# Kernel optimization log

Measured on AMD Instinct MI355X. Metric: run time of the kernel, lower is better.

Reference implementation:

```python
import jax, jax.numpy as jnp
import numpy as np

N = 200000      # num nodes
TOPK = 32       # PPR neighbors kept per node
EMB = 64        # embedding dim


def setup_inputs() -> dict:
    key = jax.random.key(0)
    k1, k2, k3 = jax.random.split(key, 3)
    emb_table = jax.random.normal(k1, (N, EMB), dtype=jnp.float32)
    wei = jax.random.uniform(k2, (N, TOPK), dtype=jnp.float32)
    nei = jax.random.randint(k3, (N, TOPK), 0, N, dtype=jnp.int64)
    return {"emb_table": emb_table, "wei": wei, "nei": nei}


def reference(emb_table, wei, nei):
    # Weight preprocessing from __init__: binary mask of nonzero ppr weights,
    # row-normalized -> uniform weights over valid neighbors.
    w = jnp.where(wei == 0, 0.0, 1.0)                       # [N, topk]
    w = w / (jnp.sum(w, axis=-1, keepdims=True) + 1e-12)    # [N, topk]
    # forward: gather neighbor embeddings, weighted sum over topk.
    top_embs = emb_table[nei]                                # [N, topk, emb]
    out = jnp.einsum("nk,nke->ne", w, top_embs)             # [N, emb]
    return out[:, None, :]                                   # [N, 1, emb] like matmul(w[:,None,:], top_embs)
```

## Files before the change

kernel.cpp:

```cpp
#include <hip/hip_runtime.h>

#define TOPK 32
#define EMB 64

__global__ __launch_bounds__(256) void absmax_partial_kernel(
    const float* __restrict__ emb, float* __restrict__ partial, int total4)
{
    const float4* src = (const float4*)emb;
    float m = 0.0f;
    for (int i = blockIdx.x * 256 + threadIdx.x; i < total4; i += gridDim.x * 256) {
        float4 v = src[i];
        m = fmaxf(m, fmaxf(fmaxf(fabsf(v.x), fabsf(v.y)),
                           fmaxf(fabsf(v.z), fabsf(v.w))));
    }
    __shared__ float red[256];
    red[threadIdx.x] = m;
    __syncthreads();
    for (int s = 128; s > 0; s >>= 1) {
        if (threadIdx.x < s) red[threadIdx.x] = fmaxf(red[threadIdx.x], red[threadIdx.x + s]);
        __syncthreads();
    }
    if (threadIdx.x == 0) partial[blockIdx.x] = red[0];
}

__global__ __launch_bounds__(256) void quant_kernel(
    const float* __restrict__ emb, signed char* __restrict__ emb8,
    const float* __restrict__ partial, float* __restrict__ stepOut,
    int n_nodes, int a_blocks)
{
    const int t = threadIdx.x;
    __shared__ float red[256];
    float m = fmaxf(fmaxf(partial[t], partial[t + 256]),
                    fmaxf(partial[t + 512], partial[t + 768]));
    red[t] = m;
    __syncthreads();
    for (int s = 128; s > 0; s >>= 1) {
        if (t < s) red[t] = fmaxf(red[t], red[t + s]);
        __syncthreads();
    }
    const float maxv = fmaxf(red[0], 1e-20f);
    const float inv_step = 127.0f / maxv;

    if ((int)blockIdx.x < a_blocks) {
        const int gid = blockIdx.x * 256 + t;
        const int total16 = n_nodes * (EMB / 16);
        if (gid < total16) {
            const float4* src = (const float4*)emb + (size_t)gid * 4;
            unsigned int w[4];
            #pragma unroll
            for (int p = 0; p < 4; ++p) {
                float4 v = src[p];
                int q0 = (int)__builtin_rintf(fminf(fmaxf(v.x * inv_step, -127.f), 127.f));
                int q1 = (int)__builtin_rintf(fminf(fmaxf(v.y * inv_step, -127.f), 127.f));
                int q2 = (int)__builtin_rintf(fminf(fmaxf(v.z * inv_step, -127.f), 127.f));
                int q3 = (int)__builtin_rintf(fminf(fmaxf(v.w * inv_step, -127.f), 127.f));
                w[p] = (unsigned int)(q0 & 0xff) | ((unsigned int)(q1 & 0xff) << 8) |
                       ((unsigned int)(q2 & 0xff) << 16) | ((unsigned int)(q3 & 0xff) << 24);
            }
            ((int4*)emb8)[gid] = make_int4((int)w[0], (int)w[1], (int)w[2], (int)w[3]);
        }
    } else {
        if (t < 4)
            ((int4*)(emb8 + (size_t)n_nodes * EMB))[t] = make_int4(0, 0, 0, 0);
        if (t == 0) stepOut[0] = maxv / 127.0f;
    }
}

__global__ __launch_bounds__(256) void gather_q8_kernel(
    const signed char* __restrict__ emb8,
    const float* __restrict__ wei,
    const int*   __restrict__ nei,
    const float* __restrict__ stepPtr,
    float*       __restrict__ out,
    int n_nodes)
{
    const int tid  = blockIdx.x * 256 + threadIdx.x;
    const int n    = tid >> 3;
    const int lane = tid & 7;
    if (n >= n_nodes) return;

    const float step = stepPtr[0];
    const long base = (long)n * TOPK;
    const int4   j4 = *(const int4*)(nei + base + lane * 4);
    const float4 w4 = *(const float4*)(wei + base + lane * 4);
    int jm[4];
    jm[0] = (w4.x != 0.0f) ? j4.x : n_nodes;
    jm[1] = (w4.y != 0.0f) ? j4.y : n_nodes;
    jm[2] = (w4.z != 0.0f) ? j4.z : n_nodes;
    jm[3] = (w4.w != 0.0f) ? j4.w : n_nodes;

    int acc[8] = {0, 0, 0, 0, 0, 0, 0, 0};
    int cnt = 0;

    #pragma unroll
    for (int t2 = 0; t2 < 4; ++t2) {
        int j[8];
        #pragma unroll
        for (int k = 0; k < 8; ++k)
            j[k] = __shfl(jm[k & 3], t2 * 2 + (k >> 2), 8);
        uint2 r[8];
        #pragma unroll
        for (int k = 0; k < 8; ++k)
            r[k] = *(const uint2*)(emb8 + (size_t)j[k] * EMB + lane * 8);
        #pragma unroll
        for (int k = 0; k < 8; ++k) {
            cnt += (j[k] != n_nodes) ? 1 : 0;
            const unsigned int x = r[k].x, y = r[k].y;
            acc[0] += (int)(signed char)(x & 0xff);
            acc[1] += (int)(signed char)((x >> 8) & 0xff);
            acc[2] += (int)(signed char)((x >> 16) & 0xff);
            acc[3] += ((int)x) >> 24;
            acc[4] += (int)(signed char)(y & 0xff);
            acc[5] += (int)(signed char)((y >> 8) & 0xff);
            acc[6] += (int)(signed char)((y >> 16) & 0xff);
            acc[7] += ((int)y) >> 24;
        }
    }

    const float mlt = step / ((float)cnt + 1e-12f);
    float4 o0, o1;
    o0.x = acc[0] * mlt; o0.y = acc[1] * mlt; o0.z = acc[2] * mlt; o0.w = acc[3] * mlt;
    o1.x = acc[4] * mlt; o1.y = acc[5] * mlt; o1.z = acc[6] * mlt; o1.w = acc[7] * mlt;
    float* op = out + (size_t)n * EMB + lane * 8;
    *(float4*)op       = o0;
    *(float4*)(op + 4) = o1;
}

__global__ __launch_bounds__(256) void pprgo_f32_kernel(
    const float* __restrict__ emb,
    const float* __restrict__ wei,
    const int*   __restrict__ nei,
    float*       __restrict__ out,
    int n_nodes)
{
    const int tid   = blockIdx.x * blockDim.x + threadIdx.x;
    const int group = tid >> 4;
    const int lane  = tid & 15;
    if (group >= n_nodes) return;
    const long base = (long)group * TOPK;
    const float w0 = wei[base + lane];
    const float w1 = wei[base + 16 + lane];
    const int   i0 = nei[base + lane];
    const int   i1 = nei[base + 16 + lane];
    const float m0 = (w0 != 0.0f) ? 1.0f : 0.0f;
    const float m1 = (w1 != 0.0f) ? 1.0f : 0.0f;
    float4 acc = make_float4(0.f, 0.f, 0.f, 0.f);
    float  cnt = 0.0f;
    #pragma unroll 8
    for (int k = 0; k < 16; ++k) {
        const int   j0 = __shfl(i0, k, 16);
        const float a0 = __shfl(m0, k, 16);
        const float4 r0 = *(const float4*)(emb + (size_t)j0 * EMB + lane * 4);
        acc.x += a0*r0.x; acc.y += a0*r0.y; acc.z += a0*r0.z; acc.w += a0*r0.w; cnt += a0;
        const int   j1 = __shfl(i1, k, 16);
        const float a1 = __shfl(m1, k, 16);
        const float4 r1 = *(const float4*)(emb + (size_t)j1 * EMB + lane * 4);
        acc.x += a1*r1.x; acc.y += a1*r1.y; acc.z += a1*r1.z; acc.w += a1*r1.w; cnt += a1;
    }
    const float sc = 1.0f / (cnt + 1e-12f);
    float4 o;
    o.x = acc.x*sc; o.y = acc.y*sc; o.z = acc.z*sc; o.w = acc.w*sc;
    *(float4*)(out + (size_t)group * EMB + lane * 4) = o;
}

extern "C" void kernel_launch(void* const* d_in, const int* in_sizes, int n_in,
                              void* d_out, int out_size, void* d_ws, size_t ws_size,
                              hipStream_t stream) {
    const float* emb = (const float*)d_in[0];
    const float* wei = (const float*)d_in[1];
    const int*   nei = (const int*)d_in[2];
    float*       out = (float*)d_out;

    const int n_nodes = in_sizes[1] / TOPK;

    const size_t emb8_bytes  = (size_t)(n_nodes + 1) * EMB;
    const size_t partial_off = (emb8_bytes + 15) & ~(size_t)15;
    const size_t need_q8     = partial_off + 1024 * sizeof(float) + 16;

    if (ws_size >= need_q8) {
        signed char* emb8   = (signed char*)d_ws;
        float*       partial = (float*)((char*)d_ws + partial_off);
        float*       stepP   = partial + 1024;

        const int total4 = n_nodes * EMB / 4;
        absmax_partial_kernel<<<1024, 256, 0, stream>>>(emb, partial, total4);

        const int a_blocks = (n_nodes * (EMB / 16) + 255) / 256;
        quant_kernel<<<a_blocks + 1, 256, 0, stream>>>(
            emb, emb8, partial, stepP, n_nodes, a_blocks);

        const int g_blocks = (n_nodes * 8 + 255) / 256;
        gather_q8_kernel<<<g_blocks, 256, 0, stream>>>(
            emb8, wei, nei, stepP, out, n_nodes);
    } else {
        const int threads = n_nodes * 16;
        pprgo_f32_kernel<<<(threads + 255) / 256, 256, 0, stream>>>(
            emb, wei, nei, out, n_nodes);
    }
}
```

Baseline: 219.4 us.

## Bucket neighbor gathers by index slice to improve cache locality

Each 8-lane group now handles four nodes and sorts their valid neighbor indices into up to eight index-range slices using shared-memory counting sort. It then gathers slice by slice, so all threads in flight touch a narrower region of the int8 table at once, which is meant to raise L2 hit rates. The cost is extra LDS atomics, a serial prefix scan done by one lane, and more registers; occupancy is capped with launch_bounds(256,6).

Result: slower. 384.5 us (+75.2%).

```diff
diff --git a/kernel.cpp b/kernel.cpp
--- a/kernel.cpp
+++ b/kernel.cpp
@@ -2,6 +2,7 @@
 
 #define TOPK 32
 #define EMB 64
+#define NPT 4
 
 __global__ __launch_bounds__(256) void absmax_partial_kernel(
     const float* __restrict__ emb, float* __restrict__ partial, int total4)
@@ -66,64 +67,140 @@
     }
 }
 
-__global__ __launch_bounds__(256) void gather_q8_kernel(
+#define ACC8(A, rx, ry) do {                                \
+    A[0] += (int)(signed char)((rx) & 0xff);                \
+    A[1] += (int)(signed char)(((rx) >> 8) & 0xff);         \
+    A[2] += (int)(signed char)(((rx) >> 16) & 0xff);        \
+    A[3] += ((int)(rx)) >> 24;                              \
+    A[4] += (int)(signed char)((ry) & 0xff);                \
+    A[5] += (int)(signed char)(((ry) >> 8) & 0xff);         \
+    A[6] += (int)(signed char)(((ry) >> 16) & 0xff);        \
+    A[7] += ((int)(ry)) >> 24; } while (0)
+
+__global__ __launch_bounds__(256, 6) void gather_q8_sliced_kernel(
     const signed char* __restrict__ emb8,
     const float* __restrict__ wei,
     const int*   __restrict__ nei,
     const float* __restrict__ stepPtr,
     float*       __restrict__ out,
-    int n_nodes)
-{
-    const int tid  = blockIdx.x * 256 + threadIdx.x;
-    const int n    = tid >> 3;
-    const int lane = tid & 7;
-    if (n >= n_nodes) return;
+    int n_nodes, int n_groups, int sshift, int nslices)
+{
+    __shared__ int s_cur[32][NPT][8];
+    __shared__ int s_lst[32][NPT][32];
+
+    const int gl   = threadIdx.x >> 3;
+    const int lane = threadIdx.x & 7;
+    const int g    = blockIdx.x * 32 + gl;
+    if (g >= n_groups) return;
+
+    #pragma unroll
+    for (int m = 0; m < NPT; ++m) s_cur[gl][m][lane] = 0;
+
+    int jm[NPT][4];
+    #pragma unroll
+    for (int m = 0; m < NPT; ++m) {
+        const int n = g + m * n_groups;
+        if (n < n_nodes) {
+            const long base = (long)n * TOPK;
+            const int4   j4 = *(const int4*)(nei + base + lane * 4);
+            const float4 w4 = *(const float4*)(wei + base + lane * 4);
+            jm[m][0] = (w4.x != 0.0f) ? j4.x : -1;
+            jm[m][1] = (w4.y != 0.0f) ? j4.y : -1;
+            jm[m][2] = (w4.z != 0.0f) ? j4.z : -1;
+            jm[m][3] = (w4.w != 0.0f) ? j4.w : -1;
+        } else {
+            jm[m][0] = jm[m][1] = jm[m][2] = jm[m][3] = -1;
+        }
+    }
+
+    #pragma unroll
+    for (int m = 0; m < NPT; ++m) {
+        #pragma unroll
+        for (int c = 0; c < 4; ++c) {
+            const int v = jm[m][c];
+            if (v >= 0) atomicAdd(&s_cur[gl][m][v >> sshift], 1);
+        }
+    }
+
+    int tot[NPT] = {0, 0, 0, 0};
+    if (lane == 0) {
+        #pragma unroll
+        for (int m = 0; m < NPT; ++m) {
+            int run = 0;
+            for (int s = 0; s < nslices; ++s) {
+                const int t = s_cur[gl][m][s];
+                s_cur[gl][m][s] = run;
+                run += t;
+            }
+            tot[m] = run;
+        }
+    }
+    #pragma unroll
+    for (int m = 0; m < NPT; ++m) tot[m] = __shfl(tot[m], 0, 8);
+
+    #pragma unroll
+    for (int m = 0; m < NPT; ++m) {
+        #pragma unroll
+        for (int c = 0; c < 4; ++c) {
+            const int v = jm[m][c];
+            if (v >= 0) {
+                const int pos = atomicAdd(&s_cur[gl][m][v >> sshift], 1);
+                s_lst[gl][m][pos] = v << 6;
+            }
+        }
+    }
+
+    int acc[NPT][8];
+    #pragma unroll
+    for (int m = 0; m < NPT; ++m)
+        #pragma unroll
+        for (int e = 0; e < 8; ++e) acc[m][e] = 0;
+
+    const signed char* ebase = emb8 + lane * 8;
+
+    for (int s = 0; s < nslices; ++s) {
+        #pragma unroll
+        for (int m = 0; m < NPT; ++m) {
+            int i = (s == 0) ? 0 : s_cur[gl][m][s - 1];
+            const int e = s_cur[gl][m][s];
+            for (; i + 4 <= e; i += 4) {
+                const int o0 = s_lst[gl][m][i];
+                const int o1 = s_lst[gl][m][i + 1];
+                const int o2 = s_lst[gl][m][i + 2];
+                const int o3 = s_lst[gl][m][i + 3];
+                const uint2 r0 = *(const uint2*)(ebase + o0);
+                const uint2 r1 = *(const uint2*)(ebase + o1);
+                const uint2 r2 = *(const uint2*)(ebase + o2);
+                const uint2 r3 = *(const uint2*)(ebase + o3);
+                ACC8(acc[m], r0.x, r0.y);
+                ACC8(acc[m], r1.x, r1.y);
+                ACC8(acc[m], r2.x, r2.y);
+                ACC8(acc[m], r3.x, r3.y);
+            }
+            for (; i < e; ++i) {
+                const int o = s_lst[gl][m][i];
+                const uint2 r = *(const uint2*)(ebase + o);
+                ACC8(acc[m], r.x, r.y);
+            }
+        }
+    }
 
     const float step = stepPtr[0];
-    const long base = (long)n * TOPK;
-    const int4   j4 = *(const int4*)(nei + base + lane * 4);
-    const float4 w4 = *(const float4*)(wei + base + lane * 4);
-    int jm[4];
-    jm[0] = (w4.x != 0.0f) ? j4.x : n_nodes;
-    jm[1] = (w4.y != 0.0f) ? j4.y : n_nodes;
-    jm[2] = (w4.z != 0.0f) ? j4.z : n_nodes;
-    jm[3] = (w4.w != 0.0f) ? j4.w : n_nodes;
-
-    int acc[8] = {0, 0, 0, 0, 0, 0, 0, 0};
-    int cnt = 0;
-
-    #pragma unroll
-    for (int t2 = 0; t2 < 4; ++t2) {
-        int j[8];
-        #pragma unroll
-        for (int k = 0; k < 8; ++k)
-            j[k] = __shfl(jm[k & 3], t2 * 2 + (k >> 2), 8);
-        uint2 r[8];
-        #pragma unroll
-        for (int k = 0; k < 8; ++k)
-            r[k] = *(const uint2*)(emb8 + (size_t)j[k] * EMB + lane * 8);
-        #pragma unroll
-        for (int k = 0; k < 8; ++k) {
-            cnt += (j[k] != n_nodes) ? 1 : 0;
-            const unsigned int x = r[k].x, y = r[k].y;
-            acc[0] += (int)(signed char)(x & 0xff);
-            acc[1] += (int)(signed char)((x >> 8) & 0xff);
-            acc[2] += (int)(signed char)((x >> 16) & 0xff);
-            acc[3] += ((int)x) >> 24;
-            acc[4] += (int)(signed char)(y & 0xff);
-            acc[5] += (int)(signed char)((y >> 8) & 0xff);
-            acc[6] += (int)(signed char)((y >> 16) & 0xff);
-            acc[7] += ((int)y) >> 24;
-        }
-    }
-
-    const float mlt = step / ((float)cnt + 1e-12f);
-    float4 o0, o1;
-    o0.x = acc[0] * mlt; o0.y = acc[1] * mlt; o0.z = acc[2] * mlt; o0.w = acc[3] * mlt;
-    o1.x = acc[4] * mlt; o1.y = acc[5] * mlt; o1.z = acc[6] * mlt; o1.w = acc[7] * mlt;
-    float* op = out + (size_t)n * EMB + lane * 8;
-    *(float4*)op       = o0;
-    *(float4*)(op + 4) = o1;
+    #pragma unroll
+    for (int m = 0; m < NPT; ++m) {
+        const int n = g + m * n_groups;
+        if (n < n_nodes) {
+            const float mlt = step / ((float)tot[m] + 1e-12f);
+            float4 o0, o1;
+            o0.x = acc[m][0] * mlt; o0.y = acc[m][1] * mlt;
+            o0.z = acc[m][2] * mlt; o0.w = acc[m][3] * mlt;
+            o1.x = acc[m][4] * mlt; o1.y = acc[m][5] * mlt;
+            o1.z = acc[m][6] * mlt; o1.w = acc[m][7] * mlt;
+            float* op = out + (size_t)n * EMB + lane * 8;
+            *(float4*)op       = o0;
+            *(float4*)(op + 4) = o1;
+        }
+    }
 }
 
 __global__ __launch_bounds__(256) void pprgo_f32_kernel(
@@ -178,7 +255,7 @@
     const size_t need_q8     = partial_off + 1024 * sizeof(float) + 16;
 
     if (ws_size >= need_q8) {
-        signed char* emb8   = (signed char*)d_ws;
+        signed char* emb8    = (signed char*)d_ws;
         float*       partial = (float*)((char*)d_ws + partial_off);
         float*       stepP   = partial + 1024;
 
@@ -189,9 +266,13 @@
         quant_kernel<<<a_blocks + 1, 256, 0, stream>>>(
             emb, emb8, partial, stepP, n_nodes, a_blocks);
 
-        const int g_blocks = (n_nodes * 8 + 255) / 256;
-        gather_q8_kernel<<<g_blocks, 256, 0, stream>>>(
-            emb8, wei, nei, stepP, out, n_nodes);
+        const int n_groups = (n_nodes + NPT - 1) / NPT;
+        int sshift = 15;
+        while (((n_nodes + (1 << sshift) - 1) >> sshift) > 8) ++sshift;
+        const int nslices = (n_nodes + (1 << sshift) - 1) >> sshift;
+        const int g_blocks = (n_groups + 31) / 32;
+        gather_q8_sliced_kernel<<<g_blocks, 256, 0, stream>>>(
+            emb8, wei, nei, stepP, out, n_nodes, n_groups, sshift, nslices);
     } else {
         const int threads = n_nodes * 16;
         pprgo_f32_kernel<<<(threads + 255) / 256, 256, 0, stream>>>(
```

## Bucket each node's neighbors by index range before gathering int8 rows

Applied to the files above, without the earlier changes.

Each 8-lane group now counting-sorts its node's valid neighbor indices into a few index-range slices, using shared-memory atomics and a prefix scan done by one lane. It then gathers the int8 rows slice by slice, so that concurrent loads across the GPU tend to hit a narrower part of the table and reuse cache better. Masked neighbors are skipped instead of being read from a zero sentinel row. The cost is extra LDS atomics, a serial scan, data-dependent loop bounds, and a smaller batch of loads in flight per iteration (4 instead of 8).

After: 225.0 us. 1.03x slower.

```diff
diff --git a/kernel.cpp b/kernel.cpp
--- a/kernel.cpp
+++ b/kernel.cpp
@@ -66,58 +66,101 @@
     }
 }
 
-__global__ __launch_bounds__(256) void gather_q8_kernel(
+#define ACC8(A, rx, ry) do {                                \
+    A[0] += (int)(signed char)((rx) & 0xff);                \
+    A[1] += (int)(signed char)(((rx) >> 8) & 0xff);         \
+    A[2] += (int)(signed char)(((rx) >> 16) & 0xff);        \
+    A[3] += ((int)(rx)) >> 24;                              \
+    A[4] += (int)(signed char)((ry) & 0xff);                \
+    A[5] += (int)(signed char)(((ry) >> 8) & 0xff);         \
+    A[6] += (int)(signed char)(((ry) >> 16) & 0xff);        \
+    A[7] += ((int)(ry)) >> 24; } while (0)
+
+__global__ __launch_bounds__(256) void gather_q8_phased_kernel(
     const signed char* __restrict__ emb8,
     const float* __restrict__ wei,
     const int*   __restrict__ nei,
     const float* __restrict__ stepPtr,
     float*       __restrict__ out,
-    int n_nodes)
-{
-    const int tid  = blockIdx.x * 256 + threadIdx.x;
-    const int n    = tid >> 3;
-    const int lane = tid & 7;
+    int n_nodes, int sshift, int nslices)
+{
+    __shared__ int s_cnt[32][9];
+    __shared__ int s_lst[32][33];
+
+    const int gl   = threadIdx.x >> 3;
+    const int lane = threadIdx.x & 7;
+    const int n    = blockIdx.x * 32 + gl;
     if (n >= n_nodes) return;
 
-    const float step = stepPtr[0];
+    if (lane < 8) {
+        s_cnt[gl][lane] = 0;
+    }
+
     const long base = (long)n * TOPK;
     const int4   j4 = *(const int4*)(nei + base + lane * 4);
     const float4 w4 = *(const float4*)(wei + base + lane * 4);
     int jm[4];
-    jm[0] = (w4.x != 0.0f) ? j4.x : n_nodes;
-    jm[1] = (w4.y != 0.0f) ? j4.y : n_nodes;
-    jm[2] = (w4.z != 0.0f) ? j4.z : n_nodes;
-    jm[3] = (w4.w != 0.0f) ? j4.w : n_nodes;
+    jm[0] = (w4.x != 0.0f) ? j4.x : -1;
+    jm[1] = (w4.y != 0.0f) ? j4.y : -1;
+    jm[2] = (w4.z != 0.0f) ? j4.z : -1;
+    jm[3] = (w4.w != 0.0f) ? j4.w : -1;
+
+    #pragma unroll
+    for (int c = 0; c < 4; ++c) {
+        const int v = jm[c];
+        if (v >= 0) atomicAdd(&s_cnt[gl][v >> sshift], 1);
+    }
+
+    int tot = 0;
+    if (lane == 0) {
+        int run = 0;
+        for (int s = 0; s < nslices; ++s) {
+            const int c = s_cnt[gl][s];
+            s_cnt[gl][s] = run;
+            run += c;
+        }
+        tot = run;
+    }
+    tot = __shfl(tot, 0, 8);
+
+    #pragma unroll
+    for (int c = 0; c < 4; ++c) {
+        const int v = jm[c];
+        if (v >= 0) {
+            const int pos = atomicAdd(&s_cnt[gl][v >> sshift], 1);
+            s_lst[gl][pos] = v << 6;
+        }
+    }
 
     int acc[8] = {0, 0, 0, 0, 0, 0, 0, 0};
-    int cnt = 0;
-
-    #pragma unroll
-    for (int t2 = 0; t2 < 4; ++t2) {
-        int j[8];
-        #pragma unroll
-        for (int k = 0; k < 8; ++k)
-            j[k] = __shfl(jm[k & 3], t2 * 2 + (k >> 2), 8);
-        uint2 r[8];
-        #pragma unroll
-        for (int k = 0; k < 8; ++k)
-            r[k] = *(const uint2*)(emb8 + (size_t)j[k] * EMB + lane * 8);
-        #pragma unroll
-        for (int k = 0; k < 8; ++k) {
-            cnt += (j[k] != n_nodes) ? 1 : 0;
-            const unsigned int x = r[k].x, y = r[k].y;
-            acc[0] += (int)(signed char)(x & 0xff);
-            acc[1] += (int)(signed char)((x >> 8) & 0xff);
-            acc[2] += (int)(signed char)((x >> 16) & 0xff);
-            acc[3] += ((int)x) >> 24;
-            acc[4] += (int)(signed char)(y & 0xff);
-            acc[5] += (int)(signed char)((y >> 8) & 0xff);
-            acc[6] += (int)(signed char)((y >> 16) & 0xff);
-            acc[7] += ((int)y) >> 24;
-        }
-    }
-
-    const float mlt = step / ((float)cnt + 1e-12f);
+    const signed char* ebase = emb8 + lane * 8;
+
+    for (int s = 0; s < nslices; ++s) {
+        int i = (s == 0) ? 0 : s_cnt[gl][s - 1];
+        const int e = s_cnt[gl][s];
+        for (; i + 4 <= e; i += 4) {
+            const int o0 = s_lst[gl][i];
+            const int o1 = s_lst[gl][i + 1];
+            const int o2 = s_lst[gl][i + 2];
+            const int o3 = s_lst[gl][i + 3];
+            const uint2 r0 = *(const uint2*)(ebase + o0);
+            const uint2 r1 = *(const uint2*)(ebase + o1);
+            const uint2 r2 = *(const uint2*)(ebase + o2);
+            const uint2 r3 = *(const uint2*)(ebase + o3);
+            ACC8(acc, r0.x, r0.y);
+            ACC8(acc, r1.x, r1.y);
+            ACC8(acc, r2.x, r2.y);
+            ACC8(acc, r3.x, r3.y);
+        }
+        for (; i < e; ++i) {
+            const int o = s_lst[gl][i];
+            const uint2 r = *(const uint2*)(ebase + o);
+            ACC8(acc, r.x, r.y);
+        }
+    }
+
+    const float step = stepPtr[0];
+    const float mlt = step / ((float)tot + 1e-12f);
     float4 o0, o1;
     o0.x = acc[0] * mlt; o0.y = acc[1] * mlt; o0.z = acc[2] * mlt; o0.w = acc[3] * mlt;
     o1.x = acc[4] * mlt; o1.y = acc[5] * mlt; o1.z = acc[6] * mlt; o1.w = acc[7] * mlt;
@@ -178,7 +221,7 @@
     const size_t need_q8     = partial_off + 1024 * sizeof(float) + 16;
 
     if (ws_size >= need_q8) {
-        signed char* emb8   = (signed char*)d_ws;
+        signed char* emb8    = (signed char*)d_ws;
         float*       partial = (float*)((char*)d_ws + partial_off);
         float*       stepP   = partial + 1024;
 
@@ -189,9 +232,12 @@
         quant_kernel<<<a_blocks + 1, 256, 0, stream>>>(
             emb, emb8, partial, stepP, n_nodes, a_blocks);
 
-        const int g_blocks = (n_nodes * 8 + 255) / 256;
-        gather_q8_kernel<<<g_blocks, 256, 0, stream>>>(
-            emb8, wei, nei, stepP, out, n_nodes);
+        int sshift = 15;
+        while (((n_nodes + (1 << sshift) - 1) >> sshift) > 8) ++sshift;
+        const int nslices = (n_nodes + (1 << sshift) - 1) >> sshift;
+        const int g_blocks = (n_nodes + 31) / 32;
+        gather_q8_phased_kernel<<<g_blocks, 256, 0, stream>>>(
+            emb8, wei, nei, stepP, out, n_nodes, sshift, nslices);
     } else {
         const int threads = n_nodes * 16;
         pprgo_f32_kernel<<<(threads + 255) / 256, 256, 0, stream>>>(
```

## Gather int8 rows slice-by-slice across a grid-wide soft barrier for cache locality

Applied to the files above, without the earlier changes.

Replaces the per-node gather kernel with a persistent 1024-block kernel. Each block first buckets the valid neighbor indices of its nodes by row slice (40000 rows) in shared memory. All blocks then walk the slices in lockstep using a spin-based global barrier with a timeout, so concurrently gathered rows come from a small region of the quantized table that can stay in L2. This aims to cut scattered off-cache reads, at the cost of shared-memory atomics, barrier stalls, lower parallelism, and reliance on all blocks being co-resident (softened by the spin limit).

New measurement: 519.8 us. 137% more time.

```diff
diff --git a/kernel.cpp b/kernel.cpp
--- a/kernel.cpp
+++ b/kernel.cpp
@@ -2,6 +2,10 @@
 
 #define TOPK 32
 #define EMB 64
+#define NBLK 1024
+#define NPG  7
+#define ROWS_SLICE 40000u
+#define MAXS 8
 
 __global__ __launch_bounds__(256) void absmax_partial_kernel(
     const float* __restrict__ emb, float* __restrict__ partial, int total4)
@@ -26,7 +30,7 @@
 __global__ __launch_bounds__(256) void quant_kernel(
     const float* __restrict__ emb, signed char* __restrict__ emb8,
     const float* __restrict__ partial, float* __restrict__ stepOut,
-    int n_nodes, int a_blocks)
+    int* __restrict__ barP, int n_nodes, int a_blocks)
 {
     const int t = threadIdx.x;
     __shared__ float red[256];
@@ -63,6 +67,139 @@
         if (t < 4)
             ((int4*)(emb8 + (size_t)n_nodes * EMB))[t] = make_int4(0, 0, 0, 0);
         if (t == 0) stepOut[0] = maxv / 127.0f;
+        if (t >= 8 && t < 8 + MAXS) barP[t - 8] = 0;
+    }
+}
+
+#define ACC8(A, rx, ry) do {                                \
+    A[0] += (int)(signed char)((rx) & 0xff);                \
+    A[1] += (int)(signed char)(((rx) >> 8) & 0xff);         \
+    A[2] += (int)(signed char)(((rx) >> 16) & 0xff);        \
+    A[3] += ((int)(rx)) >> 24;                              \
+    A[4] += (int)(signed char)((ry) & 0xff);                \
+    A[5] += (int)(signed char)(((ry) >> 8) & 0xff);         \
+    A[6] += (int)(signed char)(((ry) >> 16) & 0xff);        \
+    A[7] += ((int)(ry)) >> 24; } while (0)
+
+__global__ __launch_bounds__(256, 4) void gather_q8_coop_kernel(
+    const signed char* __restrict__ emb8,
+    const float* __restrict__ wei,
+    const int*   __restrict__ nei,
+    const float* __restrict__ stepPtr,
+    int*         __restrict__ barP,
+    float*       __restrict__ out,
+    int n_nodes, int npb, int nslices)
+{
+    __shared__ int s_cnt[32][NPG][MAXS + 1];
+    __shared__ int s_lst[32][NPG][33];
+
+    const int gl    = threadIdx.x >> 3;
+    const int lane  = threadIdx.x & 7;
+    const int nbase = blockIdx.x * npb;
+
+    #pragma unroll
+    for (int m = 0; m < NPG; ++m) {
+        s_cnt[gl][m][lane] = 0;
+        const int loc = m * 32 + gl;
+        const int n   = nbase + loc;
+        if (loc < npb && n < n_nodes) {
+            const long base = (long)n * TOPK;
+            const int4   j4 = *(const int4*)(nei + base + lane * 4);
+            const float4 w4 = *(const float4*)(wei + base + lane * 4);
+            int jm[4];
+            jm[0] = (w4.x != 0.0f) ? j4.x : -1;
+            jm[1] = (w4.y != 0.0f) ? j4.y : -1;
+            jm[2] = (w4.z != 0.0f) ? j4.z : -1;
+            jm[3] = (w4.w != 0.0f) ? j4.w : -1;
+
+            #pragma unroll
+            for (int c = 0; c < 4; ++c)
+                if (jm[c] >= 0)
+                    atomicAdd(&s_cnt[gl][m][(unsigned)jm[c] / ROWS_SLICE], 1);
+
+            if (lane == 0) {
+                int run = 0;
+                for (int s = 0; s < nslices; ++s) {
+                    const int c = s_cnt[gl][m][s];
+                    s_cnt[gl][m][s] = run;
+                    run += c;
+                }
+            }
+            #pragma unroll
+            for (int c = 0; c < 4; ++c)
+                if (jm[c] >= 0) {
+                    const int pos = atomicAdd(&s_cnt[gl][m][(unsigned)jm[c] / ROWS_SLICE], 1);
+                    s_lst[gl][m][pos] = jm[c] << 6;
+                }
+        }
+    }
+
+    int acc[NPG][8];
+    #pragma unroll
+    for (int m = 0; m < NPG; ++m)
+        #pragma unroll
+        for (int e = 0; e < 8; ++e) acc[m][e] = 0;
+
+    const signed char* ebase = emb8 + lane * 8;
+
+    for (int s = 0; s < nslices; ++s) {
+        if (s > 0) {
+            __syncthreads();
+            if (threadIdx.x == 0) {
+                __hip_atomic_fetch_add(&barP[s - 1], 1, __ATOMIC_RELAXED,
+                                       __HIP_MEMORY_SCOPE_AGENT);
+                int spins = 0;
+                while (__hip_atomic_load(&barP[s - 1], __ATOMIC_RELAXED,
+                                         __HIP_MEMORY_SCOPE_AGENT) < NBLK &&
+                       ++spins < 2000) {
+                    __builtin_amdgcn_s_sleep(2);
+                }
+            }
+            __syncthreads();
+        }
+        #pragma unroll
+        for (int m = 0; m < NPG; ++m) {
+            int i = (s == 0) ? 0 : s_cnt[gl][m][s - 1];
+            const int e = s_cnt[gl][m][s];
+            for (; i + 4 <= e; i += 4) {
+                const int o0 = s_lst[gl][m][i];
+                const int o1 = s_lst[gl][m][i + 1];
+                const int o2 = s_lst[gl][m][i + 2];
+                const int o3 = s_lst[gl][m][i + 3];
+                const uint2 r0 = *(const uint2*)(ebase + o0);
+                const uint2 r1 = *(const uint2*)(ebase + o1);
+                const uint2 r2 = *(const uint2*)(ebase + o2);
+                const uint2 r3 = *(const uint2*)(ebase + o3);
+                ACC8(acc[m], r0.x, r0.y);
+                ACC8(acc[m], r1.x, r1.y);
+                ACC8(acc[m], r2.x, r2.y);
+                ACC8(acc[m], r3.x, r3.y);
+            }
+            for (; i < e; ++i) {
+                const int o = s_lst[gl][m][i];
+                const uint2 r = *(const uint2*)(ebase + o);
+                ACC8(acc[m], r.x, r.y);
+            }
+        }
+    }
+
+    const float step = stepPtr[0];
+    #pragma unroll
+    for (int m = 0; m < NPG; ++m) {
+        const int loc = m * 32 + gl;
+        const int n   = nbase + loc;
+        if (loc < npb && n < n_nodes) {
+            const int tot = s_cnt[gl][m][nslices - 1];
+            const float mlt = step / ((float)tot + 1e-12f);
+            float4 o0, o1;
+            o0.x = acc[m][0] * mlt; o0.y = acc[m][1] * mlt;
+            o0.z = acc[m][2] * mlt; o0.w = acc[m][3] * mlt;
+            o1.x = acc[m][4] * mlt; o1.y = acc[m][5] * mlt;
+            o1.z = acc[m][6] * mlt; o1.w = acc[m][7] * mlt;
+            float* op = out + (size_t)n * EMB + lane * 8;
+            *(float4*)op       = o0;
+            *(float4*)(op + 4) = o1;
+        }
     }
 }
 
@@ -105,15 +242,7 @@
         #pragma unroll
         for (int k = 0; k < 8; ++k) {
             cnt += (j[k] != n_nodes) ? 1 : 0;
-            const unsigned int x = r[k].x, y = r[k].y;
-            acc[0] += (int)(signed char)(x & 0xff);
-            acc[1] += (int)(signed char)((x >> 8) & 0xff);
-            acc[2] += (int)(signed char)((x >> 16) & 0xff);
-            acc[3] += ((int)x) >> 24;
-            acc[4] += (int)(signed char)(y & 0xff);
-            acc[5] += (int)(signed char)((y >> 8) & 0xff);
-            acc[6] += (int)(signed char)((y >> 16) & 0xff);
-            acc[7] += ((int)y) >> 24;
+            ACC8(acc, r[k].x, r[k].y);
         }
     }
 
@@ -175,23 +304,32 @@
 
     const size_t emb8_bytes  = (size_t)(n_nodes + 1) * EMB;
     const size_t partial_off = (emb8_bytes + 15) & ~(size_t)15;
-    const size_t need_q8     = partial_off + 1024 * sizeof(float) + 16;
+    const size_t bar_off     = partial_off + 1024 * sizeof(float) + 16;
+    const size_t need_q8     = bar_off + MAXS * sizeof(int) + 16;
 
     if (ws_size >= need_q8) {
-        signed char* emb8   = (signed char*)d_ws;
+        signed char* emb8    = (signed char*)d_ws;
         float*       partial = (float*)((char*)d_ws + partial_off);
         float*       stepP   = partial + 1024;
+        int*         barP    = (int*)((char*)d_ws + bar_off);
 
         const int total4 = n_nodes * EMB / 4;
         absmax_partial_kernel<<<1024, 256, 0, stream>>>(emb, partial, total4);
 
         const int a_blocks = (n_nodes * (EMB / 16) + 255) / 256;
         quant_kernel<<<a_blocks + 1, 256, 0, stream>>>(
-            emb, emb8, partial, stepP, n_nodes, a_blocks);
-
-        const int g_blocks = (n_nodes * 8 + 255) / 256;
-        gather_q8_kernel<<<g_blocks, 256, 0, stream>>>(
-            emb8, wei, nei, stepP, out, n_nodes);
+            emb, emb8, partial, stepP, barP, n_nodes, a_blocks);
+
+        const int npb     = (n_nodes + NBLK - 1) / NBLK;
+        const int nslices = (int)((n_nodes + (int)ROWS_SLICE - 1) / (int)ROWS_SLICE);
+        if (npb <= NPG * 32 && nslices <= MAXS) {
+            gather_q8_coop_kernel<<<NBLK, 256, 0, stream>>>(
+                emb8, wei, nei, stepP, barP, out, n_nodes, npb, nslices);
+        } else {
+            const int g_blocks = (n_nodes * 8 + 255) / 256;
+            gather_q8_kernel<<<g_blocks, 256, 0, stream>>>(
+                emb8, wei, nei, stepP, out, n_nodes);
+        }
     } else {
         const int threads = n_nodes * 16;
         pprgo_f32_kernel<<<(threads + 255) / 256, 256, 0, stream>>>(
```
